# Optimization experiments

Hardware: AMD Instinct MI355X
Metric: run time of the kernel (lower is better)

Reference implementation:

```python
import jax, jax.numpy as jnp
import numpy as np

PI = float(np.pi)
EPS = 1e-6


def setup_inputs() -> dict:
    key = jax.random.key(0)
    k1, k2, k3, k4, k5 = jax.random.split(key, 5)
    B, T, D, H, Dh = 4, 4096, 1024, 16, 64
    # Xavier-uniform-like scales
    def xavier(k, shape):
        fan_in, fan_out = shape[-2], shape[-1]
        lim = float(np.sqrt(6.0 / (fan_in + fan_out)))
        return jax.random.uniform(k, shape, jnp.float32, -lim, lim)
    return {
        "query": jax.random.normal(k1, (B, T, D), jnp.float32),
        "W_Q": xavier(k2, (H, D, 1)),
        "W_K": xavier(k3, (H, D, 1)),
        "W_V": xavier(k4, (H, D, Dh)),
        "W_O": xavier(k5, (D, Dh, H)),
    }


def reference(query, W_Q, W_K, W_V, W_O):
    # q, k: [B,T,H,1]; V: [B,T,H,Dh]
    q = jnp.einsum("btd,hdo->btho", query, W_Q)
    k = jnp.einsum("btd,hdo->btho", query, W_K)
    V = jnp.einsum("btd,hde->bthe", query, W_V)
    # use_tanh path
    q = jnp.tanh(q) * (PI / 4)
    k = jnp.tanh(k) * (PI / 4)
    cos_k, sin_k = jnp.cos(k), jnp.sin(k)
    cos_q, sin_q = jnp.cos(q), jnp.sin(q)
    # causal linear attention via cumulative sums over time
    cos_KV = jnp.cumsum(cos_k * V, axis=1)  # [B,T,H,Dh]
    sin_KV = jnp.cumsum(sin_k * V, axis=1)
    heads = cos_q * cos_KV + sin_q * sin_KV  # [B,T,H,Dh]
    # epsilon normalization
    cos_K = jnp.cumsum(cos_k, axis=1)  # [B,T,H,1]
    sin_K = jnp.cumsum(sin_k, axis=1)
    denom = cos_q * cos_K + sin_q * sin_K + EPS
    heads = heads / denom
    return jnp.einsum("deh,bthe->btd", W_O, heads)
```

## Files before the change

kernel.cpp:

```cpp
#include <hip/hip_runtime.h>
#include <math.h>

#define B_ 4
#define T_ 4096
#define D_ 1024
#define H_ 16
#define DH_ 64
#define M_ (B_*T_)
#define HD_ (H_*DH_)
#define NC_ 64
#define CS_ 64
#define PI_4 0.78539816339744830962f
#define EPS_ 1e-6f

typedef short bf16x8 __attribute__((ext_vector_type(8)));
typedef float f32x4 __attribute__((ext_vector_type(4)));

static __device__ __forceinline__ unsigned short f2bf(float f) {
    unsigned u = __builtin_bit_cast(unsigned, f);
    unsigned rounding = 0x7fffu + ((u >> 16) & 1u);
    return (unsigned short)((u + rounding) >> 16);
}

#define GLDS16(gsrc, ldst) \
    __builtin_amdgcn_global_load_lds((const __attribute__((address_space(1))) void*)(gsrc), \
                                     (__attribute__((address_space(3))) void*)(ldst), 16, 0, 0)

__global__ __launch_bounds__(256) void conv_a(const float* __restrict__ in,
                                              unsigned short* __restrict__ out) {
    int i = blockIdx.x * 256 + threadIdx.x;
    float4 v = ((const float4*)in)[i];
    ushort4 o;
    o.x = f2bf(v.x); o.y = f2bf(v.y); o.z = f2bf(v.z); o.w = f2bf(v.w);
    ((ushort4*)out)[i] = o;
}

__global__ __launch_bounds__(256) void conv_wv(const float* __restrict__ WV,
                                               unsigned short* __restrict__ Bt) {
    int f = blockIdx.x * 256 + threadIdx.x;
    int n = f >> 10, k = f & 1023;
    int h = n >> 6, e = n & 63;
    Bt[f] = f2bf(WV[h * 65536 + k * 64 + e]);
}

__global__ __launch_bounds__(256) void conv_wo(const float* __restrict__ WO,
                                               unsigned short* __restrict__ Bt) {
    int f = blockIdx.x * 256 + threadIdx.x;
    int d = f >> 10, rem = f & 1023;
    int h = rem >> 6, e = rem & 63;
    Bt[f] = f2bf(WO[d * 1024 + e * 16 + h]);
}

__global__ __launch_bounds__(256) void qk_proj(const float* __restrict__ q,
                                               const float* __restrict__ wq,
                                               const float* __restrict__ wk,
                                               float* __restrict__ cq, float* __restrict__ sq,
                                               float* __restrict__ ck, float* __restrict__ sk) {
    __shared__ float row[D_];
    int m = blockIdx.x;
    int tid = threadIdx.x;
    const float4* src = (const float4*)(q + (size_t)m * D_);
    ((float4*)row)[tid] = src[tid];
    __syncthreads();
    int out = tid >> 3;
    int sub = tid & 7;
    int h = out >> 1;
    int isK = out & 1;
    const float* w = (isK ? wk : wq) + (size_t)h * D_;
    float acc = 0.f;
#pragma unroll 8
    for (int i = 0; i < 128; ++i) {
        int d = sub + (i << 3);
        acc = fmaf(row[d], w[d], acc);
    }
    acc += __shfl_xor(acc, 1);
    acc += __shfl_xor(acc, 2);
    acc += __shfl_xor(acc, 4);
    if (sub == 0) {
        float v = tanhf(acc) * PI_4;
        int b = m >> 12, t = m & (T_ - 1);
        int idx = (b * H_ + h) * T_ + t;
        float c = cosf(v), s = sinf(v);
        if (isK) { ck[idx] = c; sk[idx] = s; }
        else     { cq[idx] = c; sq[idx] = s; }
    }
}

template <int OUT_MODE>
__global__ __launch_bounds__(256) void gemm_bf16(const unsigned short* __restrict__ A,
                                                 const unsigned short* __restrict__ Bt,
                                                 float* __restrict__ Out) {
    __shared__ short As[128 * 32];
    __shared__ short Bs[128 * 32];
    const int K = 1024;
    int tid = threadIdx.x;
    int m0 = blockIdx.x * 128;
    int n0 = blockIdx.y * 128;
    int lane = tid & 63, w = tid >> 6;
    int wm = (w >> 1) * 64, wn = (w & 1) * 64;
    int r = lane & 15, g = lane >> 4;

    int srow = tid >> 2;
    int skq  = (tid & 3) * 8;

    f32x4 acc[4][4];
#pragma unroll
    for (int i = 0; i < 4; ++i)
#pragma unroll
        for (int j = 0; j < 4; ++j) acc[i][j] = (f32x4)0.f;

    const unsigned short* gA = A  + (size_t)(m0 + srow) * K + skq;
    const unsigned short* gB = Bt + (size_t)(n0 + srow) * K + skq;
    char* lA = (char*)As + tid * 16;
    char* lB = (char*)Bs + tid * 16;

    for (int k0 = 0; k0 < K; k0 += 32) {
        GLDS16(gA + k0,            lA);
        GLDS16(gA + k0 + 64 * K,   lA + 4096);
        GLDS16(gB + k0,            lB);
        GLDS16(gB + k0 + 64 * K,   lB + 4096);
        __syncthreads();

        bf16x8 af[4], bf[4];
#pragma unroll
        for (int i = 0; i < 4; ++i)
            af[i] = *(const bf16x8*)&As[(wm + i * 16 + r) * 32 + g * 8];
#pragma unroll
        for (int j = 0; j < 4; ++j)
            bf[j] = *(const bf16x8*)&Bs[(wn + j * 16 + r) * 32 + g * 8];
#pragma unroll
        for (int i = 0; i < 4; ++i)
#pragma unroll
            for (int j = 0; j < 4; ++j)
                acc[i][j] = __builtin_amdgcn_mfma_f32_16x16x32_bf16(af[i], bf[j], acc[i][j], 0, 0, 0);
        __syncthreads();
    }

#pragma unroll
    for (int i = 0; i < 4; ++i) {
#pragma unroll
        for (int j = 0; j < 4; ++j) {
#pragma unroll
            for (int q = 0; q < 4; ++q) {
                int m = m0 + wm + i * 16 + g * 4 + q;
                int n = n0 + wn + j * 16 + r;
                if (OUT_MODE == 0) {
                    int b = m >> 12, t = m & (T_ - 1);
                    int h = n >> 6, e = n & 63;
                    Out[(((size_t)(b * H_ + h) * T_ + t) << 6) + e] = acc[i][j][q];
                } else {
                    Out[(size_t)m * D_ + n] = acc[i][j][q];
                }
            }
        }
    }
}

__global__ __launch_bounds__(64) void chunk_sums(const float* __restrict__ Vt,
                                                 const float* __restrict__ ck,
                                                 const float* __restrict__ sk,
                                                 float* __restrict__ csC, float* __restrict__ csS,
                                                 float* __restrict__ kcC, float* __restrict__ kcS) {
    int blk = blockIdx.x;
    int c = blk & (NC_ - 1);
    int bh = blk >> 6;
    int e = threadIdx.x;
    const float* vbase = Vt + (((size_t)bh * T_) << 6);
    const float* ckb = ck + (size_t)bh * T_;
    const float* skb = sk + (size_t)bh * T_;
    float sc = 0.f, ss = 0.f, kc = 0.f, ks = 0.f;
    for (int i = 0; i < CS_; ++i) {
        int t = c * CS_ + i;
        float cv = ckb[t], sv = skb[t];
        float v = vbase[((size_t)t << 6) + e];
        sc = fmaf(cv, v, sc); ss = fmaf(sv, v, ss);
        kc += cv; ks += sv;
    }
    size_t oidx = ((size_t)bh * NC_ + c) * 64 + e;
    csC[oidx] = sc; csS[oidx] = ss;
    if (e == 0) { kcC[bh * NC_ + c] = kc; kcS[bh * NC_ + c] = ks; }
}

__global__ __launch_bounds__(64) void scan_chunks(float* __restrict__ csC, float* __restrict__ csS,
                                                  float* __restrict__ kcC, float* __restrict__ kcS) {
    int bh = blockIdx.x;
    int e = threadIdx.x;
    float rc = 0.f, rs = 0.f, rkc = 0.f, rks = 0.f;
    for (int c = 0; c < NC_; ++c) {
        size_t idx = ((size_t)bh * NC_ + c) * 64 + e;
        float tc = csC[idx]; csC[idx] = rc; rc += tc;
        float ts = csS[idx]; csS[idx] = rs; rs += ts;
        if (e == 0) {
            int i2 = bh * NC_ + c;
            float a = kcC[i2]; kcC[i2] = rkc; rkc += a;
            float b2 = kcS[i2]; kcS[i2] = rks; rks += b2;
        }
    }
}

__global__ __launch_bounds__(64) void finalize(const float* __restrict__ Vt,
                                               const float* __restrict__ cq, const float* __restrict__ sq,
                                               const float* __restrict__ ck, const float* __restrict__ sk,
                                               const float* __restrict__ csC, const float* __restrict__ csS,
                                               const float* __restrict__ kcC, const float* __restrict__ kcS,
                                               unsigned short* __restrict__ heads) {
    int blk = blockIdx.x;
    int c = blk & (NC_ - 1);
    int bh = blk >> 6;
    int b = bh >> 4, h = bh & 15;
    int e = threadIdx.x;
    size_t cidx = ((size_t)bh * NC_ + c) * 64 + e;
    float offc = csC[cidx], offs = csS[cidx];
    float koffc = kcC[bh * NC_ + c], koffs = kcS[bh * NC_ + c];
    const float* vbase = Vt + (((size_t)bh * T_) << 6);
    int sbase = bh * T_;
    float rc = 0.f, rs = 0.f, rkc = 0.f, rks = 0.f;
    for (int i = 0; i < CS_; ++i) {
        int t = c * CS_ + i;
        float cv = ck[sbase + t], sv = sk[sbase + t];
        float v = vbase[((size_t)t << 6) + e];
        rc = fmaf(cv, v, rc); rs = fmaf(sv, v, rs);
        rkc += cv; rks += sv;
        float cqv = cq[sbase + t], sqv = sq[sbase + t];
        float num = cqv * (offc + rc) + sqv * (offs + rs);
        float den = cqv * (koffc + rkc) + sqv * (koffs + rks) + EPS_;
        heads[(size_t)(b * T_ + t) * HD_ + h * DH_ + e] = f2bf(num / den);
    }
}

extern "C" void kernel_launch(void* const* d_in, const int* in_sizes, int n_in,
                              void* d_out, int out_size, void* d_ws, size_t ws_size,
                              hipStream_t stream) {
    const float* query = (const float*)d_in[0];
    const float* W_Q   = (const float*)d_in[1];
    const float* W_K   = (const float*)d_in[2];
    const float* W_V   = (const float*)d_in[3];
    const float* W_O   = (const float*)d_in[4];
    float* out = (float*)d_out;

    float* ws = (float*)d_ws;
    size_t off = 0;
    float* cq  = ws + off; off += (size_t)B_ * H_ * T_;
    float* sq  = ws + off; off += (size_t)B_ * H_ * T_;
    float* ck  = ws + off; off += (size_t)B_ * H_ * T_;
    float* sk  = ws + off; off += (size_t)B_ * H_ * T_;
    float* Vt  = ws + off; off += (size_t)M_ * HD_;
    float* csC = ws + off; off += (size_t)B_ * H_ * NC_ * DH_;
    float* csS = ws + off; off += (size_t)B_ * H_ * NC_ * DH_;
    float* kcC = ws + off; off += (size_t)B_ * H_ * NC_;
    float* kcS = ws + off; off += (size_t)B_ * H_ * NC_;
    unsigned short* us = (unsigned short*)(ws + off);
    size_t uoff = 0;
    unsigned short* Aq       = us + uoff; uoff += (size_t)M_ * D_;
    unsigned short* heads_bf = us + uoff; uoff += (size_t)M_ * HD_;
    unsigned short* Wv_bt    = us + uoff; uoff += (size_t)HD_ * D_;
    unsigned short* Wo_bt    = us + uoff; uoff += (size_t)D_ * HD_;

    conv_a<<<dim3(M_ * D_ / 1024), 256, 0, stream>>>(query, Aq);
    conv_wv<<<dim3(HD_ * D_ / 256), 256, 0, stream>>>(W_V, Wv_bt);
    conv_wo<<<dim3(D_ * HD_ / 256), 256, 0, stream>>>(W_O, Wo_bt);
    qk_proj<<<dim3(M_), 256, 0, stream>>>(query, W_Q, W_K, cq, sq, ck, sk);
    gemm_bf16<0><<<dim3(M_ / 128, HD_ / 128), 256, 0, stream>>>(Aq, Wv_bt, Vt);
    chunk_sums<<<dim3(B_ * H_ * NC_), 64, 0, stream>>>(Vt, ck, sk, csC, csS, kcC, kcS);
    scan_chunks<<<dim3(B_ * H_), 64, 0, stream>>>(csC, csS, kcC, kcS);
    finalize<<<dim3(B_ * H_ * NC_), 64, 0, stream>>>(Vt, cq, sq, ck, sk, csC, csS, kcC, kcS, heads_bf);
    gemm_bf16<1><<<dim3(M_ / 128, D_ / 128), 256, 0, stream>>>(heads_bf, Wo_bt, out);
}
```

Baseline: 425.9 us.

## Fuse Q/K projection and trig epilogue into the V-projection bf16 GEMM

```diff
diff --git a/kernel.cpp b/kernel.cpp
--- a/kernel.cpp
+++ b/kernel.cpp
@@ -8,6 +8,7 @@
 #define DH_ 64
 #define M_ (B_*T_)
 #define HD_ (H_*DH_)
+#define NB_ 1152
 #define NC_ 64
 #define CS_ 64
 #define PI_4 0.78539816339744830962f
@@ -43,6 +44,15 @@
     Bt[f] = f2bf(WV[h * 65536 + k * 64 + e]);
 }
 
+__global__ __launch_bounds__(256) void conv_wqk(const float* __restrict__ WQ,
+                                                const float* __restrict__ WK,
+                                                unsigned short* __restrict__ Bt) {
+    int f = blockIdx.x * 256 + threadIdx.x;
+    int row = f >> 10, k = f & 1023;
+    float v = (row < 16) ? WQ[row * 1024 + k] : WK[(row - 16) * 1024 + k];
+    Bt[(size_t)(1024 + row) * 1024 + k] = f2bf(v);
+}
+
 __global__ __launch_bounds__(256) void conv_wo(const float* __restrict__ WO,
                                                unsigned short* __restrict__ Bt) {
     int f = blockIdx.x * 256 + threadIdx.x;
@@ -51,45 +61,12 @@
     Bt[f] = f2bf(WO[d * 1024 + e * 16 + h]);
 }
 
-__global__ __launch_bounds__(256) void qk_proj(const float* __restrict__ q,
-                                               const float* __restrict__ wq,
-                                               const float* __restrict__ wk,
-                                               float* __restrict__ cq, float* __restrict__ sq,
-                                               float* __restrict__ ck, float* __restrict__ sk) {
-    __shared__ float row[D_];
-    int m = blockIdx.x;
-    int tid = threadIdx.x;
-    const float4* src = (const float4*)(q + (size_t)m * D_);
-    ((float4*)row)[tid] = src[tid];
-    __syncthreads();
-    int out = tid >> 3;
-    int sub = tid & 7;
-    int h = out >> 1;
-    int isK = out & 1;
-    const float* w = (isK ? wk : wq) + (size_t)h * D_;
-    float acc = 0.f;
-#pragma unroll 8
-    for (int i = 0; i < 128; ++i) {
-        int d = sub + (i << 3);
-        acc = fmaf(row[d], w[d], acc);
-    }
-    acc += __shfl_xor(acc, 1);
-    acc += __shfl_xor(acc, 2);
-    acc += __shfl_xor(acc, 4);
-    if (sub == 0) {
-        float v = tanhf(acc) * PI_4;
-        int b = m >> 12, t = m & (T_ - 1);
-        int idx = (b * H_ + h) * T_ + t;
-        float c = cosf(v), s = sinf(v);
-        if (isK) { ck[idx] = c; sk[idx] = s; }
-        else     { cq[idx] = c; sq[idx] = s; }
-    }
-}
-
 template <int OUT_MODE>
 __global__ __launch_bounds__(256) void gemm_bf16(const unsigned short* __restrict__ A,
                                                  const unsigned short* __restrict__ Bt,
-                                                 float* __restrict__ Out) {
+                                                 float* __restrict__ Out,
+                                                 float* __restrict__ cq, float* __restrict__ sq,
+                                                 float* __restrict__ ck, float* __restrict__ sk) {
     __shared__ short As[128 * 32];
     __shared__ short Bs[128 * 32];
     const int K = 1024;
@@ -145,9 +122,22 @@
                 int m = m0 + wm + i * 16 + g * 4 + q;
                 int n = n0 + wn + j * 16 + r;
                 if (OUT_MODE == 0) {
-                    int b = m >> 12, t = m & (T_ - 1);
-                    int h = n >> 6, e = n & 63;
-                    Out[(((size_t)(b * H_ + h) * T_ + t) << 6) + e] = acc[i][j][q];
+                    if (n < 1024) {
+                        int b = m >> 12, t = m & (T_ - 1);
+                        int h = n >> 6, e = n & 63;
+                        Out[(((size_t)(b * H_ + h) * T_ + t) << 6) + e] = acc[i][j][q];
+                    } else {
+                        int c2 = n - 1024;
+                        if (c2 < 32) {
+                            int b = m >> 12, t = m & (T_ - 1);
+                            int h = c2 & 15;
+                            float v = tanhf(acc[i][j][q]) * PI_4;
+                            float cc = cosf(v), ss = sinf(v);
+                            int idx = (b * H_ + h) * T_ + t;
+                            if (c2 < 16) { cq[idx] = cc; sq[idx] = ss; }
+                            else         { ck[idx] = cc; sk[idx] = ss; }
+                        }
+                    }
                 } else {
                     Out[(size_t)m * D_ + n] = acc[i][j][q];
                 }
@@ -253,16 +243,16 @@
     size_t uoff = 0;
     unsigned short* Aq       = us + uoff; uoff += (size_t)M_ * D_;
     unsigned short* heads_bf = us + uoff; uoff += (size_t)M_ * HD_;
-    unsigned short* Wv_bt    = us + uoff; uoff += (size_t)HD_ * D_;
+    unsigned short* Bt_v     = us + uoff; uoff += (size_t)NB_ * D_;
     unsigned short* Wo_bt    = us + uoff; uoff += (size_t)D_ * HD_;
 
     conv_a<<<dim3(M_ * D_ / 1024), 256, 0, stream>>>(query, Aq);
-    conv_wv<<<dim3(HD_ * D_ / 256), 256, 0, stream>>>(W_V, Wv_bt);
+    conv_wv<<<dim3(HD_ * D_ / 256), 256, 0, stream>>>(W_V, Bt_v);
+    conv_wqk<<<dim3(32 * D_ / 256), 256, 0, stream>>>(W_Q, W_K, Bt_v);
     conv_wo<<<dim3(D_ * HD_ / 256), 256, 0, stream>>>(W_O, Wo_bt);
-    qk_proj<<<dim3(M_), 256, 0, stream>>>(query, W_Q, W_K, cq, sq, ck, sk);
-    gemm_bf16<0><<<dim3(M_ / 128, HD_ / 128), 256, 0, stream>>>(Aq, Wv_bt, Vt);
+    gemm_bf16<0><<<dim3(M_ / 128, 9), 256, 0, stream>>>(Aq, Bt_v, Vt, cq, sq, ck, sk);
     chunk_sums<<<dim3(B_ * H_ * NC_), 64, 0, stream>>>(Vt, ck, sk, csC, csS, kcC, kcS);
     scan_chunks<<<dim3(B_ * H_), 64, 0, stream>>>(csC, csS, kcC, kcS);
     finalize<<<dim3(B_ * H_ * NC_), 64, 0, stream>>>(Vt, cq, sq, ck, sk, csC, csS, kcC, kcS, heads_bf);
-    gemm_bf16<1><<<dim3(M_ / 128, D_ / 128), 256, 0, stream>>>(heads_bf, Wo_bt, out);
-}
+    gemm_bf16<1><<<dim3(M_ / 128, D_ / 128), 256, 0, stream>>>(heads_bf, Wo_bt, out, nullptr, nullptr, nullptr, nullptr);
+}
```

Measured after the change: 660.5 us. 55.1% more time.
